# Performance work log

Hardware: AMD Instinct MI355X
Metric: run time of the kernel (lower is better)

## Reference

```python
import jax, jax.numpy as jnp
import numpy as np

B, V = 1024, 4096
CHUNK = 16  # rows of x per cdist chunk; bounds intermediate to CHUNK*B*V floats (~268MB)
T = 2.0      # module hardcodes self.T = 2 regardless of init arg
EPS = 0.1
N_ITERS = 20


def _cdist_l1(x, y):
    # torch.cdist(x, y, p=1): out[i, j] = sum_v |x[i, v] - y[j, v]| -> [B, B]
    # chunk over rows of x to avoid materializing [B, B, V]
    xc = x.reshape(B // CHUNK, CHUNK, V)
    f = lambda xb: jnp.sum(jnp.abs(xb[:, None, :] - y[None, :, :]), axis=-1)  # [CHUNK, B]
    return jax.lax.map(f, xc).reshape(B, B)


def setup_inputs() -> dict:
    key = jax.random.key(0)
    k1, k2 = jax.random.split(key)
    y_s = jax.random.normal(k1, (B, V), dtype=jnp.float32)
    y_t = jax.random.normal(k2, (B, V), dtype=jnp.float32)
    return {"y_s": y_s, "y_t": y_t}


def reference(y_s, y_t):
    p_s = jax.nn.softmax(y_s / T, axis=1)
    p_t = jax.nn.softmax(y_t / T, axis=1)
    Wxy = _cdist_l1(p_s, p_t)          # [B, B] L1 cost matrix
    K = jnp.exp(-Wxy / EPS)

    def body(P, _):
        P = P / jnp.sum(P, axis=1, keepdims=True)  # row normalize
        P = P / jnp.sum(P, axis=0, keepdims=True)  # col normalize
        return P, None

    P, _ = jax.lax.scan(body, K, None, length=N_ITERS)
    return 0.001 * jnp.sum(P * Wxy)
```

## Files before the change

kernel.cpp:

```cpp
#include <hip/hip_runtime.h>
#include <hip/hip_fp16.h>

#define BSZ 1024
#define VSZ 4096
#define NBLK 32
#define JPB 32
#define KPAD 1040

__global__ __launch_bounds__(256) void softmax_kernel(const float* __restrict__ ys,
                                                      const float* __restrict__ yt,
                                                      unsigned short* __restrict__ ps,
                                                      unsigned short* __restrict__ pt,
                                                      float* __restrict__ cpart,
                                                      unsigned* __restrict__ flags) {
    if (blockIdx.x == 0 && threadIdx.x < NBLK) flags[threadIdx.x * 32] = 0u;
    if (blockIdx.x < 3) {
        float4 z4; z4.x = z4.y = z4.z = z4.w = 0.f;
        ((float4*)cpart)[blockIdx.x * 256 + threadIdx.x] = z4;
    }
    int row = blockIdx.x;
    const float* src;
    unsigned short* dst;
    if (row < BSZ) { src = ys + (size_t)row * VSZ;         dst = ps + (size_t)row * VSZ; }
    else           { src = yt + (size_t)(row - BSZ) * VSZ; dst = pt + (size_t)(row - BSZ) * VSZ; }
    int t = threadIdx.x;
    float4 v[4];
    float m = -1e30f;
#pragma unroll
    for (int k = 0; k < 4; ++k) {
        v[k] = ((const float4*)src)[t + 256 * k];
        m = fmaxf(m, fmaxf(fmaxf(v[k].x, v[k].y), fmaxf(v[k].z, v[k].w)));
    }
#pragma unroll
    for (int d = 32; d >= 1; d >>= 1) m = fmaxf(m, __shfl_down(m, d));
    __shared__ float sred[4];
    __shared__ float sred2[4];
    int lane = t & 63, wid = t >> 6;
    if (lane == 0) sred[wid] = m;
    __syncthreads();
    m = fmaxf(fmaxf(sred[0], sred[1]), fmaxf(sred[2], sred[3]));
    const float C = 0.7213475204444817f;
    float s = 0.f;
#pragma unroll
    for (int k = 0; k < 4; ++k) {
        v[k].x = exp2f((v[k].x - m) * C);
        v[k].y = exp2f((v[k].y - m) * C);
        v[k].z = exp2f((v[k].z - m) * C);
        v[k].w = exp2f((v[k].w - m) * C);
        s += (v[k].x + v[k].y) + (v[k].z + v[k].w);
    }
#pragma unroll
    for (int d = 32; d >= 1; d >>= 1) s += __shfl_down(s, d);
    if (lane == 0) sred2[wid] = s;
    __syncthreads();
    s = (sred2[0] + sred2[1]) + (sred2[2] + sred2[3]);
    float inv = 65535.0f / s;
#pragma unroll
    for (int k = 0; k < 4; ++k) {
        union { unsigned short h[4]; uint2 u; } o;
        o.h[0] = (unsigned short)__float2uint_rn(fminf(v[k].x * inv, 65535.0f));
        o.h[1] = (unsigned short)__float2uint_rn(fminf(v[k].y * inv, 65535.0f));
        o.h[2] = (unsigned short)__float2uint_rn(fminf(v[k].z * inv, 65535.0f));
        o.h[3] = (unsigned short)__float2uint_rn(fminf(v[k].w * inv, 65535.0f));
        ((uint2*)dst)[t + 256 * k] = o.u;
    }
}

#define TSI 128
#define TSJ 64
#define LSTR 72

__global__ __launch_bounds__(256, 4) void cdist_kernel(const unsigned short* __restrict__ psh,
                                                       const unsigned short* __restrict__ pth,
                                                       float* __restrict__ spart) {
    __shared__ unsigned short sP[TSI * LSTR];
    __shared__ unsigned short sQ[TSJ * LSTR];
    const int bi = blockIdx.x;
    const int bj = blockIdx.y;
    const int bv = blockIdx.z;
    const int t = threadIdx.x;
    const int cl = t & 15;
    const int rl = t >> 4;

    const int pr = t >> 1, pc = (t & 1) * 32;
    const int qr = t >> 2, qc = (t & 3) * 16;
    const unsigned short* gP = psh + (size_t)(bi * TSI + pr) * VSZ + bv * 1024 + pc;
    const unsigned short* gQ = pth + (size_t)(bj * TSJ + qr) * VSZ + bv * 1024 + qc;
    unsigned short* lP = &sP[pr * LSTR + pc];
    unsigned short* lQ = &sQ[qr * LSTR + qc];

    unsigned acc[4][8];
#pragma unroll
    for (int w = 0; w < 4; ++w)
#pragma unroll
        for (int u = 0; u < 8; ++u) acc[w][u] = 0u;

    for (int kt = 0; kt < 16; ++kt) {
        const unsigned short* gp = gP + kt * 64;
        const unsigned short* gq = gQ + kt * 64;
        uint4 a0 = *(const uint4*)(gp + 0);
        uint4 a1 = *(const uint4*)(gp + 8);
        uint4 a2 = *(const uint4*)(gp + 16);
        uint4 a3 = *(const uint4*)(gp + 24);
        uint4 b0 = *(const uint4*)(gq + 0);
        uint4 b1 = *(const uint4*)(gq + 8);
        __syncthreads();
        *(uint4*)(lP + 0)  = a0;
        *(uint4*)(lP + 8)  = a1;
        *(uint4*)(lP + 16) = a2;
        *(uint4*)(lP + 24) = a3;
        *(uint4*)(lQ + 0)  = b0;
        *(uint4*)(lQ + 8)  = b1;
        __syncthreads();
        const unsigned short* pbase = sP + cl * LSTR;
        const unsigned short* qbase = sQ + rl * LSTR;
#pragma unroll
        for (int vv = 0; vv < 8; ++vv) {
            uint4 q[4];
#pragma unroll
            for (int w = 0; w < 4; ++w)
                q[w] = *(const uint4*)(qbase + w * 16 * LSTR + vv * 8);
#pragma unroll
            for (int h = 0; h < 4; ++h) {
                uint4 p0 = *(const uint4*)(pbase + (2 * h + 0) * 16 * LSTR + vv * 8);
                uint4 p1 = *(const uint4*)(pbase + (2 * h + 1) * 16 * LSTR + vv * 8);
#pragma unroll
                for (int w = 0; w < 4; ++w) {
                    unsigned a = acc[w][2 * h + 0];
                    a = __builtin_amdgcn_sad_u16(p0.x, q[w].x, a);
                    a = __builtin_amdgcn_sad_u16(p0.y, q[w].y, a);
                    a = __builtin_amdgcn_sad_u16(p0.z, q[w].z, a);
                    a = __builtin_amdgcn_sad_u16(p0.w, q[w].w, a);
                    acc[w][2 * h + 0] = a;
                    unsigned b = acc[w][2 * h + 1];
                    b = __builtin_amdgcn_sad_u16(p1.x, q[w].x, b);
                    b = __builtin_amdgcn_sad_u16(p1.y, q[w].y, b);
                    b = __builtin_amdgcn_sad_u16(p1.z, q[w].z, b);
                    b = __builtin_amdgcn_sad_u16(p1.w, q[w].w, b);
                    acc[w][2 * h + 1] = b;
                }
            }
        }
    }

    float* outp = spart + (size_t)bv * (BSZ * BSZ);
    const float SCL = 1.0f / 65535.0f;
#pragma unroll
    for (int w = 0; w < 4; ++w) {
        size_t jr = (size_t)(bj * TSJ + rl + 16 * w);
#pragma unroll
        for (int u = 0; u < 8; ++u) {
            int ic = bi * TSI + cl + 16 * u;
            outp[jr * BSZ + ic] = (float)acc[w][u] * SCL;
        }
    }
}

__device__ inline void grid_barrier(unsigned* flags, unsigned gen) {
    __syncthreads();
    const int t = threadIdx.x;
    if (t == 0)
        __hip_atomic_store(&flags[blockIdx.x * 32], gen, __ATOMIC_RELEASE, __HIP_MEMORY_SCOPE_AGENT);
    if (t < NBLK) {
        while (__hip_atomic_load(&flags[t * 32], __ATOMIC_RELAXED, __HIP_MEMORY_SCOPE_AGENT) < gen)
            __builtin_amdgcn_s_sleep(1);
    }
    __syncthreads();
    if (t == 0)
        (void)__hip_atomic_load(&flags[0], __ATOMIC_ACQUIRE, __HIP_MEMORY_SCOPE_AGENT);
    __syncthreads();
}

__global__ __launch_bounds__(512) void sinkhorn_kernel(const float* __restrict__ spart,
                                                       float* __restrict__ cpart,
                                                       float* __restrict__ outpart,
                                                       float* __restrict__ out,
                                                       unsigned* __restrict__ flags) {
    __shared__ __align__(16) float k_lds[JPB * KPAD];
    __shared__ __align__(16) float a_sh[BSZ];
    __shared__ float b_sh[JPB];
    __shared__ float red[JPB];
    const int z = blockIdx.x;
    const int t = threadIdx.x;
    const int j0 = z * JPB;
    const int M = BSZ * BSZ;
    const float CE = -14.426950408889634f;
#pragma unroll
    for (int m = 0; m < 16; ++m) {
        int idx = t + 512 * m;
        int row = idx >> 8;
        int col = (idx & 255) * 4;
        size_t off = (size_t)(j0 + row) * BSZ + col;
        float4 w0 = *(const float4*)(spart + off);
        float4 w1 = *(const float4*)(spart + off + M);
        float4 w2 = *(const float4*)(spart + off + 2 * M);
        float4 w3 = *(const float4*)(spart + off + 3 * M);
        float4 k;
        k.x = exp2f(((w0.x + w1.x) + (w2.x + w3.x)) * CE);
        k.y = exp2f(((w0.y + w1.y) + (w2.y + w3.y)) * CE);
        k.z = exp2f(((w0.z + w1.z) + (w2.z + w3.z)) * CE);
        k.w = exp2f(((w0.w + w1.w) + (w2.w + w3.w)) * CE);
        *(float4*)(&k_lds[row * KPAD + col]) = k;
    }
    if (t < JPB) b_sh[t] = 1.0f;
    __syncthreads();
    const int jj = t >> 4;
    const int il = t & 15;
    const int colp = (t + z * 16) & 511;
    unsigned gen = 1u;
    for (int it = 0; it < 20; ++it) {
        float* cbuf = cpart + (size_t)(it % 3) * BSZ;
        float2 s = {0.f, 0.f};
#pragma unroll
        for (int q = 0; q < JPB; ++q) {
            float2 kv = *(const float2*)(&k_lds[q * KPAD + 2 * colp]);
            float bb = b_sh[q];
            s.x += kv.x * bb; s.y += kv.y * bb;
        }
        (void)__hip_atomic_fetch_add(&cbuf[2 * colp],     s.x, __ATOMIC_RELAXED, __HIP_MEMORY_SCOPE_AGENT);
        (void)__hip_atomic_fetch_add(&cbuf[2 * colp + 1], s.y, __ATOMIC_RELAXED, __HIP_MEMORY_SCOPE_AGENT);
        grid_barrier(flags, gen++);
        float2 cv = *(const float2*)(&cbuf[2 * colp]);
        if (t < 32) cpart[(size_t)((it + 2) % 3) * BSZ + z * 32 + t] = 0.f;
        float2 ar;
        ar.x = 1.0f / cv.x; ar.y = 1.0f / cv.y;
        ((float2*)a_sh)[colp] = ar;
        __syncthreads();
        float sb = 0.f;
#pragma unroll
        for (int m2 = 0; m2 < 16; ++m2) {
            float4 kv = *(const float4*)(&k_lds[jj * KPAD + (il + 16 * m2) * 4]);
            float4 av = ((const float4*)a_sh)[il + 16 * m2];
            sb += (kv.x * av.x + kv.y * av.y) + (kv.z * av.z + kv.w * av.w);
        }
#pragma unroll
        for (int d = 8; d >= 1; d >>= 1) sb += __shfl_down(sb, d, 16);
        if (il == 0) b_sh[jj] = 1.0f / sb;
        __syncthreads();
    }
    {
        const float* wbase = spart + (size_t)(j0 + jj) * BSZ;
        float sb = 0.f;
#pragma unroll 4
        for (int m2 = 0; m2 < 16; ++m2) {
            int c4 = (il + 16 * m2) * 4;
            float4 kv = *(const float4*)(&k_lds[jj * KPAD + c4]);
            float4 av = ((const float4*)a_sh)[il + 16 * m2];
            float4 wa = *(const float4*)(wbase + c4);
            float4 wb = *(const float4*)(wbase + c4 + M);
            float4 wc = *(const float4*)(wbase + c4 + 2 * M);
            float4 wd = *(const float4*)(wbase + c4 + 3 * M);
            float4 wv;
            wv.x = (wa.x + wb.x) + (wc.x + wd.x);
            wv.y = (wa.y + wb.y) + (wc.y + wd.y);
            wv.z = (wa.z + wb.z) + (wc.z + wd.z);
            wv.w = (wa.w + wb.w) + (wc.w + wd.w);
            sb += (av.x * kv.x * wv.x + av.y * kv.y * wv.y) +
                  (av.z * kv.z * wv.z + av.w * kv.w * wv.w);
        }
#pragma unroll
        for (int d = 8; d >= 1; d >>= 1) sb += __shfl_down(sb, d, 16);
        if (il == 0) red[jj] = sb * b_sh[jj];
        __syncthreads();
        if (t == 0) {
            float ss = 0.f;
#pragma unroll
            for (int q = 0; q < JPB; ++q) ss += red[q];
            outpart[z] = ss;
        }
    }
    grid_barrier(flags, gen++);
    if (z == 0 && t == 0) {
        float ss = 0.f;
        for (int q = 0; q < NBLK; ++q) ss += outpart[q];
        out[0] = 0.001f * ss;
    }
}

extern "C" void kernel_launch(void* const* d_in, const int* in_sizes, int n_in,
                              void* d_out, int out_size, void* d_ws, size_t ws_size,
                              hipStream_t stream) {
    const float* ys = (const float*)d_in[0];
    const float* yt = (const float*)d_in[1];
    float* ws = (float*)d_ws;
    unsigned short* psh = (unsigned short*)ws;
    unsigned short* pth = (unsigned short*)(ws + 2ull * 1024 * 1024);
    float* spart   = ws + 4ull * 1024 * 1024;
    float* wt      = spart + 4ull * BSZ * BSZ;
    float* kt      = wt + (size_t)BSZ * BSZ;
    float* cpart   = kt + (size_t)BSZ * BSZ;
    float* outpart = cpart + 2ull * NBLK * BSZ;
    unsigned* flags = (unsigned*)(outpart + 128);
    float* outp    = (float*)d_out;

    softmax_kernel<<<dim3(2 * BSZ), dim3(256), 0, stream>>>(ys, yt, psh, pth, cpart, flags);
    cdist_kernel<<<dim3(8, 16, 4), dim3(256), 0, stream>>>(psh, pth, spart);
    sinkhorn_kernel<<<dim3(NBLK), dim3(512), 0, stream>>>(spart, cpart, outpart, outp, flags);
}
```

Baseline: 259.2 us.

## Fuse cdist and Sinkhorn into one persistent kernel with register-resident K

Merges the L1 cdist kernel and the Sinkhorn kernel into one 256-block launch. A grid barrier separates the cdist phase from the Sinkhorn phase, after which 32 blocks continue and the rest exit. The cdist tile grows to 128x128 with 512 threads, and each Sinkhorn thread now holds its K column slice in registers instead of an LDS K matrix. Row sums are reduced with shuffles plus a small LDS table. This removes a kernel launch and the LDS staging of K, at the cost of a 256-block spin barrier that needs all blocks co-resident, plus heavier register pressure.

```diff
diff --git a/kernel.cpp b/kernel.cpp
--- a/kernel.cpp
+++ b/kernel.cpp
@@ -5,7 +5,7 @@
 #define VSZ 4096
 #define NBLK 32
 #define JPB 32
-#define KPAD 1040
+#define FBLK 256
 
 __global__ __launch_bounds__(256) void softmax_kernel(const float* __restrict__ ys,
                                                       const float* __restrict__ yt,
@@ -13,10 +13,10 @@
                                                       unsigned short* __restrict__ pt,
                                                       float* __restrict__ cpart,
                                                       unsigned* __restrict__ flags) {
-    if (blockIdx.x == 0 && threadIdx.x < NBLK) flags[threadIdx.x * 32] = 0u;
-    if (blockIdx.x < 3) {
+    if (blockIdx.x < 32) flags[blockIdx.x * 256 + threadIdx.x] = 0u;
+    if (blockIdx.x >= 32 && blockIdx.x < 35) {
         float4 z4; z4.x = z4.y = z4.z = z4.w = 0.f;
-        ((float4*)cpart)[blockIdx.x * 256 + threadIdx.x] = z4;
+        ((float4*)cpart)[(blockIdx.x - 32) * 256 + threadIdx.x] = z4;
     }
     int row = blockIdx.x;
     const float* src;
@@ -66,103 +66,13 @@
     }
 }
 
-#define TSI 128
-#define TSJ 64
-#define LSTR 72
-
-__global__ __launch_bounds__(256, 4) void cdist_kernel(const unsigned short* __restrict__ psh,
-                                                       const unsigned short* __restrict__ pth,
-                                                       float* __restrict__ spart) {
-    __shared__ unsigned short sP[TSI * LSTR];
-    __shared__ unsigned short sQ[TSJ * LSTR];
-    const int bi = blockIdx.x;
-    const int bj = blockIdx.y;
-    const int bv = blockIdx.z;
-    const int t = threadIdx.x;
-    const int cl = t & 15;
-    const int rl = t >> 4;
-
-    const int pr = t >> 1, pc = (t & 1) * 32;
-    const int qr = t >> 2, qc = (t & 3) * 16;
-    const unsigned short* gP = psh + (size_t)(bi * TSI + pr) * VSZ + bv * 1024 + pc;
-    const unsigned short* gQ = pth + (size_t)(bj * TSJ + qr) * VSZ + bv * 1024 + qc;
-    unsigned short* lP = &sP[pr * LSTR + pc];
-    unsigned short* lQ = &sQ[qr * LSTR + qc];
-
-    unsigned acc[4][8];
-#pragma unroll
-    for (int w = 0; w < 4; ++w)
-#pragma unroll
-        for (int u = 0; u < 8; ++u) acc[w][u] = 0u;
-
-    for (int kt = 0; kt < 16; ++kt) {
-        const unsigned short* gp = gP + kt * 64;
-        const unsigned short* gq = gQ + kt * 64;
-        uint4 a0 = *(const uint4*)(gp + 0);
-        uint4 a1 = *(const uint4*)(gp + 8);
-        uint4 a2 = *(const uint4*)(gp + 16);
-        uint4 a3 = *(const uint4*)(gp + 24);
-        uint4 b0 = *(const uint4*)(gq + 0);
-        uint4 b1 = *(const uint4*)(gq + 8);
-        __syncthreads();
-        *(uint4*)(lP + 0)  = a0;
-        *(uint4*)(lP + 8)  = a1;
-        *(uint4*)(lP + 16) = a2;
-        *(uint4*)(lP + 24) = a3;
-        *(uint4*)(lQ + 0)  = b0;
-        *(uint4*)(lQ + 8)  = b1;
-        __syncthreads();
-        const unsigned short* pbase = sP + cl * LSTR;
-        const unsigned short* qbase = sQ + rl * LSTR;
-#pragma unroll
-        for (int vv = 0; vv < 8; ++vv) {
-            uint4 q[4];
-#pragma unroll
-            for (int w = 0; w < 4; ++w)
-                q[w] = *(const uint4*)(qbase + w * 16 * LSTR + vv * 8);
-#pragma unroll
-            for (int h = 0; h < 4; ++h) {
-                uint4 p0 = *(const uint4*)(pbase + (2 * h + 0) * 16 * LSTR + vv * 8);
-                uint4 p1 = *(const uint4*)(pbase + (2 * h + 1) * 16 * LSTR + vv * 8);
-#pragma unroll
-                for (int w = 0; w < 4; ++w) {
-                    unsigned a = acc[w][2 * h + 0];
-                    a = __builtin_amdgcn_sad_u16(p0.x, q[w].x, a);
-                    a = __builtin_amdgcn_sad_u16(p0.y, q[w].y, a);
-                    a = __builtin_amdgcn_sad_u16(p0.z, q[w].z, a);
-                    a = __builtin_amdgcn_sad_u16(p0.w, q[w].w, a);
-                    acc[w][2 * h + 0] = a;
-                    unsigned b = acc[w][2 * h + 1];
-                    b = __builtin_amdgcn_sad_u16(p1.x, q[w].x, b);
-                    b = __builtin_amdgcn_sad_u16(p1.y, q[w].y, b);
-                    b = __builtin_amdgcn_sad_u16(p1.z, q[w].z, b);
-                    b = __builtin_amdgcn_sad_u16(p1.w, q[w].w, b);
-                    acc[w][2 * h + 1] = b;
-                }
-            }
-        }
-    }
-
-    float* outp = spart + (size_t)bv * (BSZ * BSZ);
-    const float SCL = 1.0f / 65535.0f;
-#pragma unroll
-    for (int w = 0; w < 4; ++w) {
-        size_t jr = (size_t)(bj * TSJ + rl + 16 * w);
-#pragma unroll
-        for (int u = 0; u < 8; ++u) {
-            int ic = bi * TSI + cl + 16 * u;
-            outp[jr * BSZ + ic] = (float)acc[w][u] * SCL;
-        }
-    }
-}
-
-__device__ inline void grid_barrier(unsigned* flags, unsigned gen) {
+__device__ inline void grid_barrier_n(unsigned* flags, unsigned gen, int nblk) {
     __syncthreads();
     const int t = threadIdx.x;
     if (t == 0)
         __hip_atomic_store(&flags[blockIdx.x * 32], gen, __ATOMIC_RELEASE, __HIP_MEMORY_SCOPE_AGENT);
-    if (t < NBLK) {
-        while (__hip_atomic_load(&flags[t * 32], __ATOMIC_RELAXED, __HIP_MEMORY_SCOPE_AGENT) < gen)
+    for (int f = t; f < nblk; f += (int)blockDim.x) {
+        while (__hip_atomic_load(&flags[f * 32], __ATOMIC_RELAXED, __HIP_MEMORY_SCOPE_AGENT) < gen)
             __builtin_amdgcn_s_sleep(1);
     }
     __syncthreads();
@@ -171,109 +81,189 @@
     __syncthreads();
 }
 
-__global__ __launch_bounds__(512) void sinkhorn_kernel(const float* __restrict__ spart,
+#define LSTR 72
+
+__global__ __launch_bounds__(512, 2) void fused_kernel(const unsigned short* __restrict__ psh,
+                                                       const unsigned short* __restrict__ pth,
+                                                       float* __restrict__ spart,
                                                        float* __restrict__ cpart,
                                                        float* __restrict__ outpart,
                                                        float* __restrict__ out,
                                                        unsigned* __restrict__ flags) {
-    __shared__ __align__(16) float k_lds[JPB * KPAD];
-    __shared__ __align__(16) float a_sh[BSZ];
+    __shared__ unsigned short sP[128 * LSTR];
+    __shared__ unsigned short sQ[128 * LSTR];
+    __shared__ float redg[32 * 33];
     __shared__ float b_sh[JPB];
-    __shared__ float red[JPB];
-    const int z = blockIdx.x;
     const int t = threadIdx.x;
-    const int j0 = z * JPB;
+    const int blk = blockIdx.x;
     const int M = BSZ * BSZ;
-    const float CE = -14.426950408889634f;
-#pragma unroll
-    for (int m = 0; m < 16; ++m) {
-        int idx = t + 512 * m;
-        int row = idx >> 8;
-        int col = (idx & 255) * 4;
-        size_t off = (size_t)(j0 + row) * BSZ + col;
-        float4 w0 = *(const float4*)(spart + off);
-        float4 w1 = *(const float4*)(spart + off + M);
-        float4 w2 = *(const float4*)(spart + off + 2 * M);
-        float4 w3 = *(const float4*)(spart + off + 3 * M);
-        float4 k;
-        k.x = exp2f(((w0.x + w1.x) + (w2.x + w3.x)) * CE);
-        k.y = exp2f(((w0.y + w1.y) + (w2.y + w3.y)) * CE);
-        k.z = exp2f(((w0.z + w1.z) + (w2.z + w3.z)) * CE);
-        k.w = exp2f(((w0.w + w1.w) + (w2.w + w3.w)) * CE);
-        *(float4*)(&k_lds[row * KPAD + col]) = k;
-    }
-    if (t < JPB) b_sh[t] = 1.0f;
-    __syncthreads();
-    const int jj = t >> 4;
-    const int il = t & 15;
-    const int colp = (t + z * 16) & 511;
-    unsigned gen = 1u;
-    for (int it = 0; it < 20; ++it) {
-        float* cbuf = cpart + (size_t)(it % 3) * BSZ;
-        float2 s = {0.f, 0.f};
-#pragma unroll
+
+    {
+        const int bv = blk & 3, bj = (blk >> 2) & 7, bi = blk >> 5;
+        const int cl = t & 15;
+        const int rl = (t >> 4) & 31;
+        const int isP = (t < 256);
+        const int lt = t & 255;
+        const int sr = lt >> 1, sc = (lt & 1) * 32;
+        const unsigned short* gsrc =
+            (isP ? psh + (size_t)(bi * 128 + sr) * VSZ
+                 : pth + (size_t)(bj * 128 + sr) * VSZ) + bv * 1024 + sc;
+        unsigned short* lb = (isP ? sP : sQ) + sr * LSTR + sc;
+
+        unsigned acc[4][8];
+#pragma unroll
+        for (int w = 0; w < 4; ++w)
+#pragma unroll
+            for (int u = 0; u < 8; ++u) acc[w][u] = 0u;
+
+        for (int kt = 0; kt < 16; ++kt) {
+            const unsigned short* g = gsrc + kt * 64;
+            uint4 a0 = *(const uint4*)(g + 0);
+            uint4 a1 = *(const uint4*)(g + 8);
+            uint4 a2 = *(const uint4*)(g + 16);
+            uint4 a3 = *(const uint4*)(g + 24);
+            __syncthreads();
+            *(uint4*)(lb + 0)  = a0;
+            *(uint4*)(lb + 8)  = a1;
+            *(uint4*)(lb + 16) = a2;
+            *(uint4*)(lb + 24) = a3;
+            __syncthreads();
+            const unsigned short* pbase = sP + cl * LSTR;
+            const unsigned short* qbase = sQ + rl * LSTR;
+#pragma unroll
+            for (int vv = 0; vv < 8; ++vv) {
+                uint4 q[4];
+#pragma unroll
+                for (int w = 0; w < 4; ++w)
+                    q[w] = *(const uint4*)(qbase + w * 32 * LSTR + vv * 8);
+#pragma unroll
+                for (int h = 0; h < 4; ++h) {
+                    uint4 p0 = *(const uint4*)(pbase + (2 * h + 0) * 16 * LSTR + vv * 8);
+                    uint4 p1 = *(const uint4*)(pbase + (2 * h + 1) * 16 * LSTR + vv * 8);
+#pragma unroll
+                    for (int w = 0; w < 4; ++w) {
+                        unsigned a = acc[w][2 * h + 0];
+                        a = __builtin_amdgcn_sad_u16(p0.x, q[w].x, a);
+                        a = __builtin_amdgcn_sad_u16(p0.y, q[w].y, a);
+                        a = __builtin_amdgcn_sad_u16(p0.z, q[w].z, a);
+                        a = __builtin_amdgcn_sad_u16(p0.w, q[w].w, a);
+                        acc[w][2 * h + 0] = a;
+                        unsigned b = acc[w][2 * h + 1];
+                        b = __builtin_amdgcn_sad_u16(p1.x, q[w].x, b);
+                        b = __builtin_amdgcn_sad_u16(p1.y, q[w].y, b);
+                        b = __builtin_amdgcn_sad_u16(p1.z, q[w].z, b);
+                        b = __builtin_amdgcn_sad_u16(p1.w, q[w].w, b);
+                        acc[w][2 * h + 1] = b;
+                    }
+                }
+            }
+        }
+
+        float* outp = spart + (size_t)bv * M;
+        const float SCL = 1.0f / 65535.0f;
+#pragma unroll
+        for (int w = 0; w < 4; ++w) {
+            size_t jr = (size_t)(bj * 128 + rl + 32 * w);
+#pragma unroll
+            for (int u = 0; u < 8; ++u) {
+                int ic = bi * 128 + cl + 16 * u;
+                outp[jr * BSZ + ic] = (float)acc[w][u] * SCL;
+            }
+        }
+    }
+
+    grid_barrier_n(flags, 1u, FBLK);
+    if (blk >= NBLK) return;
+
+    {
+        const int z = blk;
+        const int colp = (t + z * 16) & 511;
+        const int c0 = 2 * colp;
+        const int j0 = z * JPB;
+        const float CE = -14.426950408889634f;
+        float kA[32], kB[32];
+#pragma unroll 8
         for (int q = 0; q < JPB; ++q) {
-            float2 kv = *(const float2*)(&k_lds[q * KPAD + 2 * colp]);
-            float bb = b_sh[q];
-            s.x += kv.x * bb; s.y += kv.y * bb;
-        }
-        (void)__hip_atomic_fetch_add(&cbuf[2 * colp],     s.x, __ATOMIC_RELAXED, __HIP_MEMORY_SCOPE_AGENT);
-        (void)__hip_atomic_fetch_add(&cbuf[2 * colp + 1], s.y, __ATOMIC_RELAXED, __HIP_MEMORY_SCOPE_AGENT);
-        grid_barrier(flags, gen++);
-        float2 cv = *(const float2*)(&cbuf[2 * colp]);
-        if (t < 32) cpart[(size_t)((it + 2) % 3) * BSZ + z * 32 + t] = 0.f;
-        float2 ar;
-        ar.x = 1.0f / cv.x; ar.y = 1.0f / cv.y;
-        ((float2*)a_sh)[colp] = ar;
+            size_t off = (size_t)(j0 + q) * BSZ + c0;
+            float2 w0 = *(const float2*)(spart + off);
+            float2 w1 = *(const float2*)(spart + off + M);
+            float2 w2 = *(const float2*)(spart + off + 2 * M);
+            float2 w3 = *(const float2*)(spart + off + 3 * M);
+            kA[q] = exp2f(((w0.x + w1.x) + (w2.x + w3.x)) * CE);
+            kB[q] = exp2f(((w0.y + w1.y) + (w2.y + w3.y)) * CE);
+        }
+        if (t < JPB) b_sh[t] = 1.0f;
         __syncthreads();
-        float sb = 0.f;
-#pragma unroll
-        for (int m2 = 0; m2 < 16; ++m2) {
-            float4 kv = *(const float4*)(&k_lds[jj * KPAD + (il + 16 * m2) * 4]);
-            float4 av = ((const float4*)a_sh)[il + 16 * m2];
-            sb += (kv.x * av.x + kv.y * av.y) + (kv.z * av.z + kv.w * av.w);
-        }
-#pragma unroll
-        for (int d = 8; d >= 1; d >>= 1) sb += __shfl_down(sb, d, 16);
-        if (il == 0) b_sh[jj] = 1.0f / sb;
-        __syncthreads();
-    }
-    {
-        const float* wbase = spart + (size_t)(j0 + jj) * BSZ;
-        float sb = 0.f;
-#pragma unroll 4
-        for (int m2 = 0; m2 < 16; ++m2) {
-            int c4 = (il + 16 * m2) * 4;
-            float4 kv = *(const float4*)(&k_lds[jj * KPAD + c4]);
-            float4 av = ((const float4*)a_sh)[il + 16 * m2];
-            float4 wa = *(const float4*)(wbase + c4);
-            float4 wb = *(const float4*)(wbase + c4 + M);
-            float4 wc = *(const float4*)(wbase + c4 + 2 * M);
-            float4 wd = *(const float4*)(wbase + c4 + 3 * M);
-            float4 wv;
-            wv.x = (wa.x + wb.x) + (wc.x + wd.x);
-            wv.y = (wa.y + wb.y) + (wc.y + wd.y);
-            wv.z = (wa.z + wb.z) + (wc.z + wd.z);
-            wv.w = (wa.w + wb.w) + (wc.w + wd.w);
-            sb += (av.x * kv.x * wv.x + av.y * kv.y * wv.y) +
-                  (av.z * kv.z * wv.z + av.w * kv.w * wv.w);
-        }
-#pragma unroll
-        for (int d = 8; d >= 1; d >>= 1) sb += __shfl_down(sb, d, 16);
-        if (il == 0) red[jj] = sb * b_sh[jj];
-        __syncthreads();
-        if (t == 0) {
+        const int g16 = t >> 4;
+        const int l16 = t & 15;
+        unsigned gen = 2u;
+        float ax = 0.f, ay = 0.f;
+        for (int it = 0; it < 20; ++it) {
+            float* cbuf = cpart + (size_t)(it % 3) * BSZ;
+            float sx = 0.f, sy = 0.f;
+#pragma unroll
+            for (int q = 0; q < JPB; ++q) {
+                float bb = b_sh[q];
+                sx += kA[q] * bb;
+                sy += kB[q] * bb;
+            }
+            (void)__hip_atomic_fetch_add(&cbuf[c0],     sx, __ATOMIC_RELAXED, __HIP_MEMORY_SCOPE_AGENT);
+            (void)__hip_atomic_fetch_add(&cbuf[c0 + 1], sy, __ATOMIC_RELAXED, __HIP_MEMORY_SCOPE_AGENT);
+            grid_barrier_n(flags, gen++, NBLK);
+            float2 cv = *(const float2*)(&cbuf[c0]);
+            if (t < 32) cpart[(size_t)((it + 2) % 3) * BSZ + z * 32 + t] = 0.f;
+            ax = 1.0f / cv.x;
+            ay = 1.0f / cv.y;
+#pragma unroll
+            for (int q = 0; q < JPB; ++q) {
+                float pq = kA[q] * ax + kB[q] * ay;
+                pq += __shfl_xor(pq, 1, 16);
+                pq += __shfl_xor(pq, 2, 16);
+                pq += __shfl_xor(pq, 4, 16);
+                pq += __shfl_xor(pq, 8, 16);
+                if (l16 == 0) redg[g16 * 33 + q] = pq;
+            }
+            __syncthreads();
+            if (t < JPB) {
+                float s8 = 0.f;
+#pragma unroll
+                for (int k = 0; k < 32; ++k) s8 += redg[k * 33 + t];
+                b_sh[t] = 1.0f / s8;
+            }
+            __syncthreads();
+        }
+        {
+            float fin = 0.f;
+#pragma unroll 8
+            for (int q = 0; q < JPB; ++q) {
+                size_t off = (size_t)(j0 + q) * BSZ + c0;
+                float2 w0 = *(const float2*)(spart + off);
+                float2 w1 = *(const float2*)(spart + off + M);
+                float2 w2 = *(const float2*)(spart + off + 2 * M);
+                float2 w3 = *(const float2*)(spart + off + 3 * M);
+                float wx = (w0.x + w1.x) + (w2.x + w3.x);
+                float wy = (w0.y + w1.y) + (w2.y + w3.y);
+                fin += b_sh[q] * (kA[q] * ax * wx + kB[q] * ay * wy);
+            }
+            fin += __shfl_xor(fin, 1, 16);
+            fin += __shfl_xor(fin, 2, 16);
+            fin += __shfl_xor(fin, 4, 16);
+            fin += __shfl_xor(fin, 8, 16);
+            if (l16 == 0) redg[g16 * 33] = fin;
+            __syncthreads();
+            if (t == 0) {
+                float ss = 0.f;
+#pragma unroll
+                for (int k = 0; k < 32; ++k) ss += redg[k * 33];
+                outpart[z] = ss;
+            }
+        }
+        grid_barrier_n(flags, gen++, NBLK);
+        if (z == 0 && t == 0) {
             float ss = 0.f;
-#pragma unroll
-            for (int q = 0; q < JPB; ++q) ss += red[q];
-            outpart[z] = ss;
-        }
-    }
-    grid_barrier(flags, gen++);
-    if (z == 0 && t == 0) {
-        float ss = 0.f;
-        for (int q = 0; q < NBLK; ++q) ss += outpart[q];
-        out[0] = 0.001f * ss;
+            for (int q = 0; q < NBLK; ++q) ss += outpart[q];
+            out[0] = 0.001f * ss;
+        }
     }
 }
 
@@ -294,6 +284,5 @@
     float* outp    = (float*)d_out;
 
     softmax_kernel<<<dim3(2 * BSZ), dim3(256), 0, stream>>>(ys, yt, psh, pth, cpart, flags);
-    cdist_kernel<<<dim3(8, 16, 4), dim3(256), 0, stream>>>(psh, pth, spart);
-    sinkhorn_kernel<<<dim3(NBLK), dim3(512), 0, stream>>>(spart, cpart, outpart, outp, flags);
-}
+    fused_kernel<<<dim3(FBLK), dim3(512), 0, stream>>>(psh, pth, spart, cpart, outpart, outp, flags);
+}
```

New measurement: 348.6 us. 34.5% more time.

## Fuse softmax and cdist into one persistent kernel with grid barrier

Applied to the files above, without the earlier changes.

Merges the softmax kernel and the cdist kernel into one 512-block launch. Each block softmax-quantizes four rows, then all blocks meet at a software grid barrier before running their cdist tile. This removes one kernel launch and the gap between launches. In exchange it adds a hipMemsetAsync to reset the barrier flags, and it relies on all 512 blocks being resident at once to avoid deadlock.

```diff
diff --git a/kernel.cpp b/kernel.cpp
--- a/kernel.cpp
+++ b/kernel.cpp
@@ -6,79 +6,99 @@
 #define NBLK 32
 #define JPB 32
 #define KPAD 1040
-
-__global__ __launch_bounds__(256) void softmax_kernel(const float* __restrict__ ys,
-                                                      const float* __restrict__ yt,
-                                                      unsigned short* __restrict__ ps,
-                                                      unsigned short* __restrict__ pt,
-                                                      float* __restrict__ cpart,
-                                                      unsigned* __restrict__ flags) {
-    if (blockIdx.x == 0 && threadIdx.x < NBLK) flags[threadIdx.x * 32] = 0u;
-    if (blockIdx.x < 3) {
-        float4 z4; z4.x = z4.y = z4.z = z4.w = 0.f;
-        ((float4*)cpart)[blockIdx.x * 256 + threadIdx.x] = z4;
-    }
-    int row = blockIdx.x;
-    const float* src;
-    unsigned short* dst;
-    if (row < BSZ) { src = ys + (size_t)row * VSZ;         dst = ps + (size_t)row * VSZ; }
-    else           { src = yt + (size_t)(row - BSZ) * VSZ; dst = pt + (size_t)(row - BSZ) * VSZ; }
-    int t = threadIdx.x;
-    float4 v[4];
-    float m = -1e30f;
-#pragma unroll
-    for (int k = 0; k < 4; ++k) {
-        v[k] = ((const float4*)src)[t + 256 * k];
-        m = fmaxf(m, fmaxf(fmaxf(v[k].x, v[k].y), fmaxf(v[k].z, v[k].w)));
-    }
-#pragma unroll
-    for (int d = 32; d >= 1; d >>= 1) m = fmaxf(m, __shfl_down(m, d));
-    __shared__ float sred[4];
-    __shared__ float sred2[4];
-    int lane = t & 63, wid = t >> 6;
-    if (lane == 0) sred[wid] = m;
-    __syncthreads();
-    m = fmaxf(fmaxf(sred[0], sred[1]), fmaxf(sred[2], sred[3]));
-    const float C = 0.7213475204444817f;
-    float s = 0.f;
-#pragma unroll
-    for (int k = 0; k < 4; ++k) {
-        v[k].x = exp2f((v[k].x - m) * C);
-        v[k].y = exp2f((v[k].y - m) * C);
-        v[k].z = exp2f((v[k].z - m) * C);
-        v[k].w = exp2f((v[k].w - m) * C);
-        s += (v[k].x + v[k].y) + (v[k].z + v[k].w);
-    }
-#pragma unroll
-    for (int d = 32; d >= 1; d >>= 1) s += __shfl_down(s, d);
-    if (lane == 0) sred2[wid] = s;
-    __syncthreads();
-    s = (sred2[0] + sred2[1]) + (sred2[2] + sred2[3]);
-    float inv = 65535.0f / s;
-#pragma unroll
-    for (int k = 0; k < 4; ++k) {
-        union { unsigned short h[4]; uint2 u; } o;
-        o.h[0] = (unsigned short)__float2uint_rn(fminf(v[k].x * inv, 65535.0f));
-        o.h[1] = (unsigned short)__float2uint_rn(fminf(v[k].y * inv, 65535.0f));
-        o.h[2] = (unsigned short)__float2uint_rn(fminf(v[k].z * inv, 65535.0f));
-        o.h[3] = (unsigned short)__float2uint_rn(fminf(v[k].w * inv, 65535.0f));
-        ((uint2*)dst)[t + 256 * k] = o.u;
-    }
+#define FBLK 512
+
+__device__ inline void grid_barrier_n(unsigned* flags, unsigned gen, int nblk) {
+    __syncthreads();
+    const int t = threadIdx.x;
+    if (t == 0)
+        __hip_atomic_store(&flags[blockIdx.x * 32], gen, __ATOMIC_RELEASE, __HIP_MEMORY_SCOPE_AGENT);
+    for (int f = t; f < nblk; f += (int)blockDim.x) {
+        while (__hip_atomic_load(&flags[f * 32], __ATOMIC_RELAXED, __HIP_MEMORY_SCOPE_AGENT) < gen)
+            __builtin_amdgcn_s_sleep(1);
+    }
+    __syncthreads();
+    if (t == 0)
+        (void)__hip_atomic_load(&flags[0], __ATOMIC_ACQUIRE, __HIP_MEMORY_SCOPE_AGENT);
+    __syncthreads();
 }
 
 #define TSI 128
 #define TSJ 64
 #define LSTR 72
 
-__global__ __launch_bounds__(256, 4) void cdist_kernel(const unsigned short* __restrict__ psh,
-                                                       const unsigned short* __restrict__ pth,
-                                                       float* __restrict__ spart) {
+__global__ __launch_bounds__(256, 4) void fused_sc_kernel(const float* __restrict__ ys,
+                                                          const float* __restrict__ yt,
+                                                          unsigned short* __restrict__ psh,
+                                                          unsigned short* __restrict__ pth,
+                                                          float* __restrict__ spart,
+                                                          float* __restrict__ cpart,
+                                                          unsigned* __restrict__ flagsA,
+                                                          unsigned* __restrict__ flagsB) {
+    const int t = threadIdx.x;
+    const int blk = blockIdx.x;
+    __shared__ float sred[4];
+    __shared__ float sred2[4];
+
+    if (blk == 0 && t < NBLK) flagsB[t * 32] = 0u;
+    if (blk >= 32 && blk < 35) {
+        float4 z4; z4.x = z4.y = z4.z = z4.w = 0.f;
+        ((float4*)cpart)[(blk - 32) * 256 + t] = z4;
+    }
+    const float C = 0.7213475204444817f;
+    for (int r = 0; r < 4; ++r) {
+        int row = blk * 4 + r;
+        const float* src;
+        unsigned short* dst;
+        if (row < BSZ) { src = ys + (size_t)row * VSZ;         dst = psh + (size_t)row * VSZ; }
+        else           { src = yt + (size_t)(row - BSZ) * VSZ; dst = pth + (size_t)(row - BSZ) * VSZ; }
+        float4 v[4];
+        float m = -1e30f;
+#pragma unroll
+        for (int k = 0; k < 4; ++k) {
+            v[k] = ((const float4*)src)[t + 256 * k];
+            m = fmaxf(m, fmaxf(fmaxf(v[k].x, v[k].y), fmaxf(v[k].z, v[k].w)));
+        }
+#pragma unroll
+        for (int d = 32; d >= 1; d >>= 1) m = fmaxf(m, __shfl_down(m, d));
+        int lane = t & 63, wid = t >> 6;
+        if (lane == 0) sred[wid] = m;
+        __syncthreads();
+        m = fmaxf(fmaxf(sred[0], sred[1]), fmaxf(sred[2], sred[3]));
+        float s = 0.f;
+#pragma unroll
+        for (int k = 0; k < 4; ++k) {
+            v[k].x = exp2f((v[k].x - m) * C);
+            v[k].y = exp2f((v[k].y - m) * C);
+            v[k].z = exp2f((v[k].z - m) * C);
+            v[k].w = exp2f((v[k].w - m) * C);
+            s += (v[k].x + v[k].y) + (v[k].z + v[k].w);
+        }
+#pragma unroll
+        for (int d = 32; d >= 1; d >>= 1) s += __shfl_down(s, d);
+        if (lane == 0) sred2[wid] = s;
+        __syncthreads();
+        s = (sred2[0] + sred2[1]) + (sred2[2] + sred2[3]);
+        float inv = 65535.0f / s;
+#pragma unroll
+        for (int k = 0; k < 4; ++k) {
+            union { unsigned short h[4]; uint2 u; } o;
+            o.h[0] = (unsigned short)__float2uint_rn(fminf(v[k].x * inv, 65535.0f));
+            o.h[1] = (unsigned short)__float2uint_rn(fminf(v[k].y * inv, 65535.0f));
+            o.h[2] = (unsigned short)__float2uint_rn(fminf(v[k].z * inv, 65535.0f));
+            o.h[3] = (unsigned short)__float2uint_rn(fminf(v[k].w * inv, 65535.0f));
+            ((uint2*)dst)[t + 256 * k] = o.u;
+        }
+        __syncthreads();
+    }
+
+    grid_barrier_n(flagsA, 1u, FBLK);
+
     __shared__ unsigned short sP[TSI * LSTR];
     __shared__ unsigned short sQ[TSJ * LSTR];
-    const int bi = blockIdx.x;
-    const int bj = blockIdx.y;
-    const int bv = blockIdx.z;
-    const int t = threadIdx.x;
+    const int bi = blk & 7;
+    const int bj = (blk >> 3) & 15;
+    const int bv = blk >> 7;
     const int cl = t & 15;
     const int rl = t >> 4;
 
@@ -290,10 +310,12 @@
     float* kt      = wt + (size_t)BSZ * BSZ;
     float* cpart   = kt + (size_t)BSZ * BSZ;
     float* outpart = cpart + 2ull * NBLK * BSZ;
-    unsigned* flags = (unsigned*)(outpart + 128);
+    unsigned* flagsB = (unsigned*)(outpart + 128);
+    unsigned* flagsA = flagsB + NBLK * 32;
     float* outp    = (float*)d_out;
 
-    softmax_kernel<<<dim3(2 * BSZ), dim3(256), 0, stream>>>(ys, yt, psh, pth, cpart, flags);
-    cdist_kernel<<<dim3(8, 16, 4), dim3(256), 0, stream>>>(psh, pth, spart);
-    sinkhorn_kernel<<<dim3(NBLK), dim3(512), 0, stream>>>(spart, cpart, outpart, outp, flags);
-}
+    (void)hipMemsetAsync(flagsA, 0, FBLK * 32 * sizeof(unsigned), stream);
+    fused_sc_kernel<<<dim3(FBLK), dim3(256), 0, stream>>>(ys, yt, psh, pth, spart,
+                                                          cpart, flagsA, flagsB);
+    sinkhorn_kernel<<<dim3(NBLK), dim3(512), 0, stream>>>(spart, cpart, outpart, outp, flagsB);
+}
```

After: 274.1 us. 1.06x slower.

## Fuse cdist and Sinkhorn into one persistent kernel with 128 Sinkhorn blocks

Applied to the files above, without the earlier changes.

Merges the L1 cdist kernel and the Sinkhorn kernel into one 512-block launch separated by a grid barrier. After the barrier, 128 blocks of 8 rows each run the Sinkhorn iterations instead of 32 blocks of 32 rows. Column sums go through four separate atomic buffers to cut contention, and row sums use wave shuffles. The final cost is recovered from K with a log instead of re-reading the spart partials. This removes a launch boundary and spreads Sinkhorn over more CUs, at the price of a 512-block grid barrier that assumes all blocks are co-resident, more barrier participants per iteration, and small precision loss from the log(exp) round-trip.

```diff
diff --git a/kernel.cpp b/kernel.cpp
--- a/kernel.cpp
+++ b/kernel.cpp
@@ -3,9 +3,13 @@
 
 #define BSZ 1024
 #define VSZ 4096
-#define NBLK 32
-#define JPB 32
-#define KPAD 1040
+#define NSB 128
+#define RPB 8
+#define KP  1040
+#define FBLK 512
+#define TSI 128
+#define TSJ 64
+#define LSTR 72
 
 __global__ __launch_bounds__(256) void softmax_kernel(const float* __restrict__ ys,
                                                       const float* __restrict__ yt,
@@ -13,10 +17,10 @@
                                                       unsigned short* __restrict__ pt,
                                                       float* __restrict__ cpart,
                                                       unsigned* __restrict__ flags) {
-    if (blockIdx.x == 0 && threadIdx.x < NBLK) flags[threadIdx.x * 32] = 0u;
-    if (blockIdx.x < 3) {
+    if (blockIdx.x < 64) flags[blockIdx.x * 256 + threadIdx.x] = 0u;
+    else if (blockIdx.x < 76) {
         float4 z4; z4.x = z4.y = z4.z = z4.w = 0.f;
-        ((float4*)cpart)[blockIdx.x * 256 + threadIdx.x] = z4;
+        ((float4*)cpart)[(blockIdx.x - 64) * 256 + threadIdx.x] = z4;
     }
     int row = blockIdx.x;
     const float* src;
@@ -66,103 +70,13 @@
     }
 }
 
-#define TSI 128
-#define TSJ 64
-#define LSTR 72
-
-__global__ __launch_bounds__(256, 4) void cdist_kernel(const unsigned short* __restrict__ psh,
-                                                       const unsigned short* __restrict__ pth,
-                                                       float* __restrict__ spart) {
-    __shared__ unsigned short sP[TSI * LSTR];
-    __shared__ unsigned short sQ[TSJ * LSTR];
-    const int bi = blockIdx.x;
-    const int bj = blockIdx.y;
-    const int bv = blockIdx.z;
-    const int t = threadIdx.x;
-    const int cl = t & 15;
-    const int rl = t >> 4;
-
-    const int pr = t >> 1, pc = (t & 1) * 32;
-    const int qr = t >> 2, qc = (t & 3) * 16;
-    const unsigned short* gP = psh + (size_t)(bi * TSI + pr) * VSZ + bv * 1024 + pc;
-    const unsigned short* gQ = pth + (size_t)(bj * TSJ + qr) * VSZ + bv * 1024 + qc;
-    unsigned short* lP = &sP[pr * LSTR + pc];
-    unsigned short* lQ = &sQ[qr * LSTR + qc];
-
-    unsigned acc[4][8];
-#pragma unroll
-    for (int w = 0; w < 4; ++w)
-#pragma unroll
-        for (int u = 0; u < 8; ++u) acc[w][u] = 0u;
-
-    for (int kt = 0; kt < 16; ++kt) {
-        const unsigned short* gp = gP + kt * 64;
-        const unsigned short* gq = gQ + kt * 64;
-        uint4 a0 = *(const uint4*)(gp + 0);
-        uint4 a1 = *(const uint4*)(gp + 8);
-        uint4 a2 = *(const uint4*)(gp + 16);
-        uint4 a3 = *(const uint4*)(gp + 24);
-        uint4 b0 = *(const uint4*)(gq + 0);
-        uint4 b1 = *(const uint4*)(gq + 8);
-        __syncthreads();
-        *(uint4*)(lP + 0)  = a0;
-        *(uint4*)(lP + 8)  = a1;
-        *(uint4*)(lP + 16) = a2;
-        *(uint4*)(lP + 24) = a3;
-        *(uint4*)(lQ + 0)  = b0;
-        *(uint4*)(lQ + 8)  = b1;
-        __syncthreads();
-        const unsigned short* pbase = sP + cl * LSTR;
-        const unsigned short* qbase = sQ + rl * LSTR;
-#pragma unroll
-        for (int vv = 0; vv < 8; ++vv) {
-            uint4 q[4];
-#pragma unroll
-            for (int w = 0; w < 4; ++w)
-                q[w] = *(const uint4*)(qbase + w * 16 * LSTR + vv * 8);
-#pragma unroll
-            for (int h = 0; h < 4; ++h) {
-                uint4 p0 = *(const uint4*)(pbase + (2 * h + 0) * 16 * LSTR + vv * 8);
-                uint4 p1 = *(const uint4*)(pbase + (2 * h + 1) * 16 * LSTR + vv * 8);
-#pragma unroll
-                for (int w = 0; w < 4; ++w) {
-                    unsigned a = acc[w][2 * h + 0];
-                    a = __builtin_amdgcn_sad_u16(p0.x, q[w].x, a);
-                    a = __builtin_amdgcn_sad_u16(p0.y, q[w].y, a);
-                    a = __builtin_amdgcn_sad_u16(p0.z, q[w].z, a);
-                    a = __builtin_amdgcn_sad_u16(p0.w, q[w].w, a);
-                    acc[w][2 * h + 0] = a;
-                    unsigned b = acc[w][2 * h + 1];
-                    b = __builtin_amdgcn_sad_u16(p1.x, q[w].x, b);
-                    b = __builtin_amdgcn_sad_u16(p1.y, q[w].y, b);
-                    b = __builtin_amdgcn_sad_u16(p1.z, q[w].z, b);
-                    b = __builtin_amdgcn_sad_u16(p1.w, q[w].w, b);
-                    acc[w][2 * h + 1] = b;
-                }
-            }
-        }
-    }
-
-    float* outp = spart + (size_t)bv * (BSZ * BSZ);
-    const float SCL = 1.0f / 65535.0f;
-#pragma unroll
-    for (int w = 0; w < 4; ++w) {
-        size_t jr = (size_t)(bj * TSJ + rl + 16 * w);
-#pragma unroll
-        for (int u = 0; u < 8; ++u) {
-            int ic = bi * TSI + cl + 16 * u;
-            outp[jr * BSZ + ic] = (float)acc[w][u] * SCL;
-        }
-    }
-}
-
-__device__ inline void grid_barrier(unsigned* flags, unsigned gen) {
+__device__ inline void grid_barrier_n(unsigned* flags, unsigned gen, int nblk) {
     __syncthreads();
     const int t = threadIdx.x;
     if (t == 0)
         __hip_atomic_store(&flags[blockIdx.x * 32], gen, __ATOMIC_RELEASE, __HIP_MEMORY_SCOPE_AGENT);
-    if (t < NBLK) {
-        while (__hip_atomic_load(&flags[t * 32], __ATOMIC_RELAXED, __HIP_MEMORY_SCOPE_AGENT) < gen)
+    for (int f = t; f < nblk; f += (int)blockDim.x) {
+        while (__hip_atomic_load(&flags[f * 32], __ATOMIC_RELAXED, __HIP_MEMORY_SCOPE_AGENT) < gen)
             __builtin_amdgcn_s_sleep(1);
     }
     __syncthreads();
@@ -171,26 +85,112 @@
     __syncthreads();
 }
 
-__global__ __launch_bounds__(512) void sinkhorn_kernel(const float* __restrict__ spart,
-                                                       float* __restrict__ cpart,
-                                                       float* __restrict__ outpart,
-                                                       float* __restrict__ out,
-                                                       unsigned* __restrict__ flags) {
-    __shared__ __align__(16) float k_lds[JPB * KPAD];
-    __shared__ __align__(16) float a_sh[BSZ];
-    __shared__ float b_sh[JPB];
-    __shared__ float red[JPB];
-    const int z = blockIdx.x;
+__global__ __launch_bounds__(256, 4) void fused_cs_kernel(const unsigned short* __restrict__ psh,
+                                                          const unsigned short* __restrict__ pth,
+                                                          float* __restrict__ spart,
+                                                          float* __restrict__ cpart,
+                                                          float* __restrict__ outpart,
+                                                          float* __restrict__ out,
+                                                          unsigned* __restrict__ flags) {
+    __shared__ __align__(16) unsigned char smem[RPB * KP * 4];
+    __shared__ float b_sh[RPB];
+    __shared__ float redsm[4][RPB];
     const int t = threadIdx.x;
-    const int j0 = z * JPB;
+    const int blk = blockIdx.x;
     const int M = BSZ * BSZ;
+
+    {
+        unsigned short* sP = (unsigned short*)smem;
+        unsigned short* sQ = (unsigned short*)(smem + TSI * LSTR * 2);
+        const int bi = blk & 7;
+        const int bj = (blk >> 3) & 15;
+        const int bv = blk >> 7;
+        const int cl = t & 15;
+        const int rl = t >> 4;
+        const int pr = t >> 1, pc = (t & 1) * 32;
+        const int qr = t >> 2, qc = (t & 3) * 16;
+        const unsigned short* gP = psh + (size_t)(bi * TSI + pr) * VSZ + bv * 1024 + pc;
+        const unsigned short* gQ = pth + (size_t)(bj * TSJ + qr) * VSZ + bv * 1024 + qc;
+        unsigned short* lP = &sP[pr * LSTR + pc];
+        unsigned short* lQ = &sQ[qr * LSTR + qc];
+
+        unsigned acc[4][8];
+#pragma unroll
+        for (int w = 0; w < 4; ++w)
+#pragma unroll
+            for (int u = 0; u < 8; ++u) acc[w][u] = 0u;
+
+        for (int kt = 0; kt < 16; ++kt) {
+            const unsigned short* gp = gP + kt * 64;
+            const unsigned short* gq = gQ + kt * 64;
+            uint4 a0 = *(const uint4*)(gp + 0);
+            uint4 a1 = *(const uint4*)(gp + 8);
+            uint4 a2 = *(const uint4*)(gp + 16);
+            uint4 a3 = *(const uint4*)(gp + 24);
+            uint4 b0 = *(const uint4*)(gq + 0);
+            uint4 b1 = *(const uint4*)(gq + 8);
+            __syncthreads();
+            *(uint4*)(lP + 0)  = a0;
+            *(uint4*)(lP + 8)  = a1;
+            *(uint4*)(lP + 16) = a2;
+            *(uint4*)(lP + 24) = a3;
+            *(uint4*)(lQ + 0)  = b0;
+            *(uint4*)(lQ + 8)  = b1;
+            __syncthreads();
+            const unsigned short* pbase = sP + cl * LSTR;
+            const unsigned short* qbase = sQ + rl * LSTR;
+#pragma unroll
+            for (int vv = 0; vv < 8; ++vv) {
+                uint4 q[4];
+#pragma unroll
+                for (int w = 0; w < 4; ++w)
+                    q[w] = *(const uint4*)(qbase + w * 16 * LSTR + vv * 8);
+#pragma unroll
+                for (int h = 0; h < 4; ++h) {
+                    uint4 p0 = *(const uint4*)(pbase + (2 * h + 0) * 16 * LSTR + vv * 8);
+                    uint4 p1 = *(const uint4*)(pbase + (2 * h + 1) * 16 * LSTR + vv * 8);
+#pragma unroll
+                    for (int w = 0; w < 4; ++w) {
+                        unsigned a = acc[w][2 * h + 0];
+                        a = __builtin_amdgcn_sad_u16(p0.x, q[w].x, a);
+                        a = __builtin_amdgcn_sad_u16(p0.y, q[w].y, a);
+                        a = __builtin_amdgcn_sad_u16(p0.z, q[w].z, a);
+                        a = __builtin_amdgcn_sad_u16(p0.w, q[w].w, a);
+                        acc[w][2 * h + 0] = a;
+                        unsigned b = acc[w][2 * h + 1];
+                        b = __builtin_amdgcn_sad_u16(p1.x, q[w].x, b);
+                        b = __builtin_amdgcn_sad_u16(p1.y, q[w].y, b);
+                        b = __builtin_amdgcn_sad_u16(p1.z, q[w].z, b);
+                        b = __builtin_amdgcn_sad_u16(p1.w, q[w].w, b);
+                        acc[w][2 * h + 1] = b;
+                    }
+                }
+            }
+        }
+
+        float* outp = spart + (size_t)bv * M;
+        const float SCL = 1.0f / 65535.0f;
+#pragma unroll
+        for (int w = 0; w < 4; ++w) {
+            size_t jr = (size_t)(bj * TSJ + rl + 16 * w);
+#pragma unroll
+            for (int u = 0; u < 8; ++u) {
+                int ic = bi * TSI + cl + 16 * u;
+                outp[jr * BSZ + ic] = (float)acc[w][u] * SCL;
+            }
+        }
+    }
+
+    grid_barrier_n(flags, 1u, FBLK);
+    if (blk >= NSB) return;
+
+    float* k_lds = (float*)smem;
+    const int z = blk;
+    const int j0 = z * RPB;
     const float CE = -14.426950408889634f;
 #pragma unroll
-    for (int m = 0; m < 16; ++m) {
-        int idx = t + 512 * m;
-        int row = idx >> 8;
-        int col = (idx & 255) * 4;
-        size_t off = (size_t)(j0 + row) * BSZ + col;
+    for (int q = 0; q < RPB; ++q) {
+        size_t off = (size_t)(j0 + q) * BSZ + 4 * t;
         float4 w0 = *(const float4*)(spart + off);
         float4 w1 = *(const float4*)(spart + off + M);
         float4 w2 = *(const float4*)(spart + off + 2 * M);
@@ -200,79 +200,87 @@
         k.y = exp2f(((w0.y + w1.y) + (w2.y + w3.y)) * CE);
         k.z = exp2f(((w0.z + w1.z) + (w2.z + w3.z)) * CE);
         k.w = exp2f(((w0.w + w1.w) + (w2.w + w3.w)) * CE);
-        *(float4*)(&k_lds[row * KPAD + col]) = k;
-    }
-    if (t < JPB) b_sh[t] = 1.0f;
-    __syncthreads();
-    const int jj = t >> 4;
-    const int il = t & 15;
-    const int colp = (t + z * 16) & 511;
-    unsigned gen = 1u;
+        *(float4*)(&k_lds[q * KP + 4 * t]) = k;
+    }
+    if (t < RPB) b_sh[t] = 1.0f;
+    __syncthreads();
+    const int colq = (t + 2 * z) & 255;
+    const int c0 = 4 * colq;
+    const int g = z >> 5;
+    unsigned gen = 2u;
+    float4 a4 = {0.f, 0.f, 0.f, 0.f};
     for (int it = 0; it < 20; ++it) {
-        float* cbuf = cpart + (size_t)(it % 3) * BSZ;
-        float2 s = {0.f, 0.f};
-#pragma unroll
-        for (int q = 0; q < JPB; ++q) {
-            float2 kv = *(const float2*)(&k_lds[q * KPAD + 2 * colp]);
+        float* cbuf = cpart + (size_t)(it % 3) * 4096;
+        float4 s = {0.f, 0.f, 0.f, 0.f};
+#pragma unroll
+        for (int q = 0; q < RPB; ++q) {
+            float4 k = *(const float4*)(&k_lds[q * KP + c0]);
             float bb = b_sh[q];
-            s.x += kv.x * bb; s.y += kv.y * bb;
-        }
-        (void)__hip_atomic_fetch_add(&cbuf[2 * colp],     s.x, __ATOMIC_RELAXED, __HIP_MEMORY_SCOPE_AGENT);
-        (void)__hip_atomic_fetch_add(&cbuf[2 * colp + 1], s.y, __ATOMIC_RELAXED, __HIP_MEMORY_SCOPE_AGENT);
-        grid_barrier(flags, gen++);
-        float2 cv = *(const float2*)(&cbuf[2 * colp]);
-        if (t < 32) cpart[(size_t)((it + 2) % 3) * BSZ + z * 32 + t] = 0.f;
-        float2 ar;
-        ar.x = 1.0f / cv.x; ar.y = 1.0f / cv.y;
-        ((float2*)a_sh)[colp] = ar;
+            s.x += k.x * bb; s.y += k.y * bb; s.z += k.z * bb; s.w += k.w * bb;
+        }
+        float* dc = cbuf + g * 1024 + c0;
+        (void)__hip_atomic_fetch_add(dc + 0, s.x, __ATOMIC_RELAXED, __HIP_MEMORY_SCOPE_AGENT);
+        (void)__hip_atomic_fetch_add(dc + 1, s.y, __ATOMIC_RELAXED, __HIP_MEMORY_SCOPE_AGENT);
+        (void)__hip_atomic_fetch_add(dc + 2, s.z, __ATOMIC_RELAXED, __HIP_MEMORY_SCOPE_AGENT);
+        (void)__hip_atomic_fetch_add(dc + 3, s.w, __ATOMIC_RELAXED, __HIP_MEMORY_SCOPE_AGENT);
+        grid_barrier_n(flags, gen++, NSB);
+        float4 c0v = *(const float4*)(cbuf + 0 * 1024 + c0);
+        float4 c1v = *(const float4*)(cbuf + 1 * 1024 + c0);
+        float4 c2v = *(const float4*)(cbuf + 2 * 1024 + c0);
+        float4 c3v = *(const float4*)(cbuf + 3 * 1024 + c0);
+        if (t < 32) cpart[(size_t)((it + 2) % 3) * 4096 + z * 32 + t] = 0.f;
+        a4.x = 1.0f / ((c0v.x + c1v.x) + (c2v.x + c3v.x));
+        a4.y = 1.0f / ((c0v.y + c1v.y) + (c2v.y + c3v.y));
+        a4.z = 1.0f / ((c0v.z + c1v.z) + (c2v.z + c3v.z));
+        a4.w = 1.0f / ((c0v.w + c1v.w) + (c2v.w + c3v.w));
+#pragma unroll
+        for (int q = 0; q < RPB; ++q) {
+            float4 k = *(const float4*)(&k_lds[q * KP + c0]);
+            float pq = (k.x * a4.x + k.y * a4.y) + (k.z * a4.z + k.w * a4.w);
+            pq += __shfl_xor(pq, 1);
+            pq += __shfl_xor(pq, 2);
+            pq += __shfl_xor(pq, 4);
+            pq += __shfl_xor(pq, 8);
+            pq += __shfl_xor(pq, 16);
+            pq += __shfl_xor(pq, 32);
+            if ((t & 63) == 0) redsm[t >> 6][q] = pq;
+        }
         __syncthreads();
-        float sb = 0.f;
-#pragma unroll
-        for (int m2 = 0; m2 < 16; ++m2) {
-            float4 kv = *(const float4*)(&k_lds[jj * KPAD + (il + 16 * m2) * 4]);
-            float4 av = ((const float4*)a_sh)[il + 16 * m2];
-            sb += (kv.x * av.x + kv.y * av.y) + (kv.z * av.z + kv.w * av.w);
-        }
-#pragma unroll
-        for (int d = 8; d >= 1; d >>= 1) sb += __shfl_down(sb, d, 16);
-        if (il == 0) b_sh[jj] = 1.0f / sb;
+        if (t < RPB) {
+            float sb = (redsm[0][t] + redsm[1][t]) + (redsm[2][t] + redsm[3][t]);
+            b_sh[t] = 1.0f / sb;
+        }
         __syncthreads();
     }
     {
-        const float* wbase = spart + (size_t)(j0 + jj) * BSZ;
-        float sb = 0.f;
-#pragma unroll 4
-        for (int m2 = 0; m2 < 16; ++m2) {
-            int c4 = (il + 16 * m2) * 4;
-            float4 kv = *(const float4*)(&k_lds[jj * KPAD + c4]);
-            float4 av = ((const float4*)a_sh)[il + 16 * m2];
-            float4 wa = *(const float4*)(wbase + c4);
-            float4 wb = *(const float4*)(wbase + c4 + M);
-            float4 wc = *(const float4*)(wbase + c4 + 2 * M);
-            float4 wd = *(const float4*)(wbase + c4 + 3 * M);
-            float4 wv;
-            wv.x = (wa.x + wb.x) + (wc.x + wd.x);
-            wv.y = (wa.y + wb.y) + (wc.y + wd.y);
-            wv.z = (wa.z + wb.z) + (wc.z + wd.z);
-            wv.w = (wa.w + wb.w) + (wc.w + wd.w);
-            sb += (av.x * kv.x * wv.x + av.y * kv.y * wv.y) +
-                  (av.z * kv.z * wv.z + av.w * kv.w * wv.w);
-        }
-#pragma unroll
-        for (int d = 8; d >= 1; d >>= 1) sb += __shfl_down(sb, d, 16);
-        if (il == 0) red[jj] = sb * b_sh[jj];
+        const float ICE = 1.0f / CE;
+        float fin = 0.f;
+#pragma unroll
+        for (int q = 0; q < RPB; ++q) {
+            float4 k = *(const float4*)(&k_lds[q * KP + c0]);
+            float4 w;
+            w.x = log2f(k.x) * ICE;
+            w.y = log2f(k.y) * ICE;
+            w.z = log2f(k.z) * ICE;
+            w.w = log2f(k.w) * ICE;
+            fin += b_sh[q] * ((a4.x * k.x * w.x + a4.y * k.y * w.y) +
+                              (a4.z * k.z * w.z + a4.w * k.w * w.w));
+        }
+        fin += __shfl_xor(fin, 1);
+        fin += __shfl_xor(fin, 2);
+        fin += __shfl_xor(fin, 4);
+        fin += __shfl_xor(fin, 8);
+        fin += __shfl_xor(fin, 16);
+        fin += __shfl_xor(fin, 32);
+        if ((t & 63) == 0) redsm[t >> 6][0] = fin;
         __syncthreads();
-        if (t == 0) {
-            float ss = 0.f;
-#pragma unroll
-            for (int q = 0; q < JPB; ++q) ss += red[q];
-            outpart[z] = ss;
-        }
-    }
-    grid_barrier(flags, gen++);
+        if (t == 0)
+            outpart[z] = (redsm[0][0] + redsm[1][0]) + (redsm[2][0] + redsm[3][0]);
+    }
+    grid_barrier_n(flags, gen++, NSB);
     if (z == 0 && t == 0) {
         float ss = 0.f;
-        for (int q = 0; q < NBLK; ++q) ss += outpart[q];
+        for (int q = 0; q < NSB; ++q) ss += outpart[q];
         out[0] = 0.001f * ss;
     }
 }
@@ -286,14 +294,12 @@
     unsigned short* psh = (unsigned short*)ws;
     unsigned short* pth = (unsigned short*)(ws + 2ull * 1024 * 1024);
     float* spart   = ws + 4ull * 1024 * 1024;
-    float* wt      = spart + 4ull * BSZ * BSZ;
-    float* kt      = wt + (size_t)BSZ * BSZ;
-    float* cpart   = kt + (size_t)BSZ * BSZ;
-    float* outpart = cpart + 2ull * NBLK * BSZ;
-    unsigned* flags = (unsigned*)(outpart + 128);
+    float* cpart   = spart + 4ull * BSZ * BSZ;
+    float* outpart = cpart + 3ull * 4096;
+    unsigned* flags = (unsigned*)(outpart + 256);
     float* outp    = (float*)d_out;
 
     softmax_kernel<<<dim3(2 * BSZ), dim3(256), 0, stream>>>(ys, yt, psh, pth, cpart, flags);
-    cdist_kernel<<<dim3(8, 16, 4), dim3(256), 0, stream>>>(psh, pth, spart);
-    sinkhorn_kernel<<<dim3(NBLK), dim3(512), 0, stream>>>(spart, cpart, outpart, outp, flags);
+    fused_cs_kernel<<<dim3(FBLK), dim3(256), 0, stream>>>(psh, pth, spart, cpart,
+                                                          outpart, outp, flags);
 }
```

Result: slower. 366.3 us (+41.3%).
